# Performance work log

Measured on AMD Instinct MI355X. Metric: run time of the kernel, lower is better.

The kernel has to match this reference:

```python
import jax, jax.numpy as jnp
import numpy as np

N = 51200      # total nodes
E = 1638400    # total edges (avg degree 32)
G = 512        # graphs in batch
IN = 16        # input node features
H = 4          # heads
C = 32         # channels per head
HC = H * C     # 128, concat output width
SLOPE = 0.2    # LeakyReLU negative slope
BN_EPS = 1e-5


def _glorot(k, shape, fan):
    return jax.random.normal(k, shape, jnp.float32) / np.sqrt(fan).astype(np.float32)


def setup_inputs() -> dict:
    key = jax.random.key(0)
    ks = jax.random.split(key, 32)
    inp = {}
    inp['x'] = jax.random.normal(ks[0], (N, IN), jnp.float32)
    inp['edge_index'] = jax.random.randint(ks[1], (2, E), 0, N)
    inp['batch'] = jnp.sort(jax.random.randint(ks[2], (N,), 0, G))
    # GATv2 layer 1 (IN -> H*C)
    inp['l1_Wl'] = _glorot(ks[3], (IN, HC), IN)
    inp['l1_bl'] = jnp.zeros((HC,), jnp.float32)
    inp['l1_Wr'] = _glorot(ks[4], (IN, HC), IN)
    inp['l1_br'] = jnp.zeros((HC,), jnp.float32)
    inp['l1_att'] = _glorot(ks[5], (H, C), C)
    inp['l1_bias'] = jnp.zeros((HC,), jnp.float32)
    # GATv2 layer 2 (HC -> H*C)
    inp['l2_Wl'] = _glorot(ks[6], (HC, HC), HC)
    inp['l2_bl'] = jnp.zeros((HC,), jnp.float32)
    inp['l2_Wr'] = _glorot(ks[7], (HC, HC), HC)
    inp['l2_br'] = jnp.zeros((HC,), jnp.float32)
    inp['l2_att'] = _glorot(ks[8], (H, C), C)
    inp['l2_bias'] = jnp.zeros((HC,), jnp.float32)
    # MLP head (HC -> HC -> HC -> 2) with BatchNorm (eval mode, running stats 0/1)
    inp['fc1_W'] = _glorot(ks[9], (HC, HC), HC)
    inp['fc1_b'] = jnp.zeros((HC,), jnp.float32)
    inp['bn1_g'] = jnp.ones((HC,), jnp.float32)
    inp['bn1_b'] = jnp.zeros((HC,), jnp.float32)
    inp['fc2_W'] = _glorot(ks[10], (HC, HC), HC)
    inp['fc2_b'] = jnp.zeros((HC,), jnp.float32)
    inp['bn2_g'] = jnp.ones((HC,), jnp.float32)
    inp['bn2_b'] = jnp.zeros((HC,), jnp.float32)
    inp['fc3_W'] = _glorot(ks[11], (HC, 2), HC)
    inp['fc3_b'] = jnp.zeros((2,), jnp.float32)
    return inp


def gatv2_conv(x, src, dst, Wl, bl, Wr, br, att, bias):
    # PyG GATv2Conv (share_weights=False, concat=True), eval mode (no dropout).
    xl = (x @ Wl + bl).reshape(-1, H, C)  # source transform  [N,H,C]
    xr = (x @ Wr + br).reshape(-1, H, C)  # target transform  [N,H,C]
    e = jax.nn.leaky_relu(xl[src] + xr[dst], SLOPE)   # [E,H,C]
    score = jnp.einsum('ehc,hc->eh', e, att)          # [E,H]
    # segment softmax over edges sharing the same target node
    m = jax.ops.segment_max(score, dst, num_segments=N)
    ex = jnp.exp(score - m[dst])
    denom = jax.ops.segment_sum(ex, dst, num_segments=N)
    alpha = ex / (denom[dst] + 1e-16)                 # [E,H]
    out = jax.ops.segment_sum(xl[src] * alpha[:, :, None], dst, num_segments=N)
    return out.reshape(-1, HC) + bias


def reference(x, edge_index, batch,
              l1_Wl, l1_bl, l1_Wr, l1_br, l1_att, l1_bias,
              l2_Wl, l2_bl, l2_Wr, l2_br, l2_att, l2_bias,
              fc1_W, fc1_b, bn1_g, bn1_b,
              fc2_W, fc2_b, bn2_g, bn2_b,
              fc3_W, fc3_b):
    src, dst = edge_index[0], edge_index[1]
    h = jax.nn.relu(gatv2_conv(x, src, dst, l1_Wl, l1_bl, l1_Wr, l1_br, l1_att, l1_bias))
    h = jax.nn.relu(gatv2_conv(h, src, dst, l2_Wl, l2_bl, l2_Wr, l2_br, l2_att, l2_bias))
    # global mean pool over graphs
    s = jax.ops.segment_sum(h, batch, num_segments=G)
    cnt = jax.ops.segment_sum(jnp.ones((N,), h.dtype), batch, num_segments=G)
    g = s / jnp.maximum(cnt, 1.0)[:, None]            # [G,HC]
    # MLP head; BatchNorm1d in eval mode with running_mean=0, running_var=1
    def bn(z, gamma, beta):
        return z * (gamma / np.sqrt(1.0 + BN_EPS).astype(np.float32)) + beta
    g = jax.nn.relu(bn(g @ fc1_W + fc1_b, bn1_g, bn1_b))
    g = jax.nn.relu(bn(g @ fc2_W + fc2_b, bn2_g, bn2_b))
    return g @ fc3_W + fc3_b                          # [G,2]
```

## Files before the change

### kernel.cpp

```cpp
#include <hip/hip_runtime.h>
#include <math.h>

#define NN 51200
#define EE 1638400
#define GG 512
#define INF 16
#define HCC 128
#define NB 400
#define TILE 4096
#define NBLK (NN / 4)

typedef float vf2 __attribute__((ext_vector_type(2)));
typedef short v8s __attribute__((ext_vector_type(8)));
typedef float v4f __attribute__((ext_vector_type(4)));
#define FMA2 __builtin_elementwise_fma
#define MIN2 __builtin_elementwise_min
#define MAX2 __builtin_elementwise_max


__device__ __forceinline__ int wave_incl_scan(int v, int lane) {
#pragma unroll
    for (int d = 1; d < 64; d <<= 1) {
        int y = __shfl_up(v, d);
        if (lane >= d) v += y;
    }
    return v;
}

__device__ __forceinline__ unsigned short bf16_rtne(float f) {
    unsigned u = __builtin_bit_cast(unsigned, f);
    unsigned r = u + 0x7FFFu + ((u >> 16) & 1u);
    return (unsigned short)(r >> 16);
}

__global__ __launch_bounds__(256) void k_hist(const int* __restrict__ ei,
                                              int* __restrict__ bcnt) {
    __shared__ int h[NB];
    for (int i = threadIdx.x; i < NB; i += 256) h[i] = 0;
    __syncthreads();
    int e0 = blockIdx.x * TILE;
#pragma unroll
    for (int s = 0; s < 16; s++) {
        int d = ei[EE + e0 + s * 256 + threadIdx.x];
        atomicAdd(&h[d >> 7], 1);
    }
    __syncthreads();
    for (int i = threadIdx.x; i < NB; i += 256)
        if (h[i]) atomicAdd(&bcnt[i], h[i]);
}

__global__ __launch_bounds__(512) void k_scan2(const int* __restrict__ bcnt,
                                               int* __restrict__ bbase,
                                               int* __restrict__ gcur,
                                               int* __restrict__ rowptr) {
    __shared__ int sc[512];
    int t = threadIdx.x;
    int v = (t < NB) ? bcnt[t] : 0;
    sc[t] = v;
    __syncthreads();
    for (int off = 1; off < 512; off <<= 1) {
        int u = (t >= off) ? sc[t - off] : 0;
        __syncthreads();
        sc[t] += u;
        __syncthreads();
    }
    if (t < NB) { int ex = sc[t] - v; bbase[t] = ex; gcur[t] = ex; }
    if (t == 0) { bbase[NB] = EE; rowptr[NN] = EE; }
}

__global__ __launch_bounds__(512) void k_binlin1(const int* __restrict__ ei,
                                                 int* __restrict__ gcur,
                                                 unsigned* __restrict__ binned,
                                                 const float* __restrict__ x,
                                                 const float* __restrict__ Wl,
                                                 const float* __restrict__ bl,
                                                 const float* __restrict__ Wr,
                                                 const float* __restrict__ br,
                                                 float* __restrict__ xl,
                                                 float* __restrict__ xr,
                                                 const float* __restrict__ W2l,
                                                 const float* __restrict__ W2r,
                                                 unsigned short* __restrict__ Bhi,
                                                 unsigned short* __restrict__ Blo) {
    __shared__ int h[512];
    __shared__ int lexcl[NB], lcur[NB], baseg[NB];
    __shared__ unsigned stage[TILE];
    __shared__ int wsum[8];
    __shared__ float sx[4][INF];
    int t = threadIdx.x;
    if (blockIdx.x < NB) {
        int lane = t & 63, w = t >> 6;
        h[t] = 0;
        __syncthreads();
        int e0 = blockIdx.x * TILE;
        int sv[8], dv[8];
#pragma unroll
        for (int s = 0; s < 8; s++) {
            int e = e0 + s * 512 + t;
            sv[s] = ei[e];
            dv[s] = ei[EE + e];
            atomicAdd(&h[dv[s] >> 7], 1);
        }
        __syncthreads();
        int myh = h[t];
        int incl = wave_incl_scan(myh, lane);
        if (lane == 63) wsum[w] = incl;
        __syncthreads();
        int woff = 0;
        for (int i = 0; i < w; i++) woff += wsum[i];
        incl += woff;
        if (t < NB) {
            int ex = incl - myh;
            lexcl[t] = ex;
            lcur[t] = ex;
            baseg[t] = atomicAdd(&gcur[t], myh);
        }
        __syncthreads();
#pragma unroll
        for (int s = 0; s < 8; s++) {
            int b = dv[s] >> 7;
            int r = atomicAdd(&lcur[b], 1);
            stage[r] = (unsigned)sv[s] | ((unsigned)dv[s] << 16);
        }
        __syncthreads();
#pragma unroll
        for (int s = 0; s < 8; s++) {
            int idx = s * 512 + t;
            unsigned p = stage[idx];
            int b = (int)(p >> 23);
            binned[baseg[b] + idx - lexcl[b]] = p;
        }
    } else if (blockIdx.x < NB + NN / 4) {
        int bid = blockIdx.x - NB;
        int j = t & 127;
        int ty = t >> 7;
        int row = bid * 4 + ty;
        if (t < 64) {
            sx[t >> 4][t & 15] = x[(size_t)(bid * 4 + (t >> 4)) * INF + (t & 15)];
        }
        __syncthreads();
        float al = bl[j], ar = br[j];
#pragma unroll
        for (int k = 0; k < INF; k++) {
            float xv = sx[ty][k];
            al = fmaf(xv, Wl[k * HCC + j], al);
            ar = fmaf(xv, Wr[k * HCC + j], ar);
        }
        size_t s = ((size_t)(j >> 5) * NN + row) * 32 + (j & 31);
        xl[s] = al;
        xr[s] = ar;
    } else {
        int gt = (blockIdx.x - NB - NN / 4) * 512 + t;
        int ks = gt >> 10;
        int rem = gt & 1023;
        int nt = rem >> 6;
        int lane = rem & 63;
        int n = nt * 16 + (lane & 15);
        int kbase = ks * 32 + (lane >> 4) * 8;
        const float* src = (n < 128) ? (W2l + n) : (W2r + n - 128);
        unsigned short hi8[8], lo8[8];
#pragma unroll
        for (int j = 0; j < 8; j++) {
            float v = src[(size_t)(kbase + j) * HCC];
            unsigned short hb = bf16_rtne(v);
            float hf = __builtin_bit_cast(float, (unsigned)hb << 16);
            hi8[j] = hb;
            lo8[j] = bf16_rtne(v - hf);
        }
        size_t idx = (size_t)gt * 8;
#pragma unroll
        for (int j = 0; j < 8; j++) { Bhi[idx + j] = hi8[j]; Blo[idx + j] = lo8[j]; }
    }
}

__global__ __launch_bounds__(256) void k_csr(const unsigned* __restrict__ binned,
                                             const int* __restrict__ bbase,
                                             int* __restrict__ rowptr,
                                             int* __restrict__ col) {
    int b = blockIdx.x;
    int base = bbase[b];
    int cnt = bbase[b + 1] - base;
    __shared__ int nh[1024], ncur[1024];
    __shared__ int wsum[4];
    int t = threadIdx.x;
    int lane = t & 63, w = t >> 6;
#pragma unroll
    for (int i = 0; i < 4; i++) nh[t + 256 * i] = 0;
    __syncthreads();
    for (int e = t; e < cnt; e += 256) {
        unsigned p = binned[base + e];
        unsigned src = p & 0xFFFFu;
        int key = (int)(((p >> 16) & 127u) << 3) | (int)(src >> 13);
        atomicAdd(&nh[key], 1);
    }
    __syncthreads();
    int c0 = nh[4 * t + 0], c1 = nh[4 * t + 1], c2 = nh[4 * t + 2], c3 = nh[4 * t + 3];
    int tot = ((c0 + c1) + (c2 + c3));
    int incl = wave_incl_scan(tot, lane);
    if (lane == 63) wsum[w] = incl;
    __syncthreads();
    int woff = 0;
    for (int i = 0; i < w; i++) woff += wsum[i];
    int tex = incl + woff - tot;
    ncur[4 * t + 0] = base + tex;
    ncur[4 * t + 1] = base + tex + c0;
    ncur[4 * t + 2] = base + tex + c0 + c1;
    ncur[4 * t + 3] = base + tex + c0 + c1 + c2;
    if ((t & 1) == 0) rowptr[(b << 7) + (t >> 1)] = base + tex;
    __syncthreads();
    for (int e = t; e < cnt; e += 256) {
        unsigned p = binned[base + e];
        unsigned src = p & 0xFFFFu;
        int key = (int)(((p >> 16) & 127u) << 3) | (int)(src >> 13);
        int r = atomicAdd(&ncur[key], 1);
        col[r] = (int)src;
    }
}

__global__ __launch_bounds__(256) void k_lin2(const float* __restrict__ hin,
                                              const unsigned short* __restrict__ Bhi,
                                              const unsigned short* __restrict__ Blo,
                                              const float* __restrict__ bl,
                                              const float* __restrict__ br,
                                              float* __restrict__ outl,
                                              float* __restrict__ outr) {
    const int tid = threadIdx.x;
    const int wv = tid >> 6;
    const int lane = tid & 63;
    const int m = lane & 15;
    const int quad = lane >> 4;
    const int r0 = blockIdx.x * 64 + wv * 16;
    const float* arow = hin + (size_t)(r0 + m) * HCC + quad * 8;
    const v8s* bh = (const v8s*)Bhi;
    const v8s* bo = (const v8s*)Blo;

    v4f acc[16];
#pragma unroll
    for (int nt = 0; nt < 16; nt++) acc[nt] = (v4f){0.f, 0.f, 0.f, 0.f};

#pragma unroll
    for (int ks = 0; ks < 4; ks++) {
        const float4 av0 = *(const float4*)(arow + ks * 32);
        const float4 av1 = *(const float4*)(arow + ks * 32 + 4);
        const float af[8] = {av0.x, av0.y, av0.z, av0.w, av1.x, av1.y, av1.z, av1.w};
        v8s ahi, alo;
#pragma unroll
        for (int e = 0; e < 8; e++) {
            unsigned short hb = bf16_rtne(af[e]);
            float hf = __builtin_bit_cast(float, (unsigned)hb << 16);
            ahi[e] = (short)hb;
            alo[e] = (short)bf16_rtne(af[e] - hf);
        }
        const int base = ks * 16 * 64 + lane;
#pragma unroll
        for (int nt = 0; nt < 16; nt++) {
            v8s bhv = bh[base + nt * 64];
            v8s blv = bo[base + nt * 64];
            acc[nt] = __builtin_amdgcn_mfma_f32_16x16x32_bf16(ahi, bhv, acc[nt], 0, 0, 0);
            acc[nt] = __builtin_amdgcn_mfma_f32_16x16x32_bf16(ahi, blv, acc[nt], 0, 0, 0);
            acc[nt] = __builtin_amdgcn_mfma_f32_16x16x32_bf16(alo, bhv, acc[nt], 0, 0, 0);
        }
    }
#pragma unroll
    for (int nt = 0; nt < 16; nt++) {
        int n = nt * 16 + m;
        int c = n & 127;
        float bv = (n < 128) ? bl[c] : br[c];
        float* outp = ((n < 128) ? outl : outr) + (size_t)(c >> 5) * NN * 32 + (c & 31);
#pragma unroll
        for (int r = 0; r < 4; r++) {
            int row = r0 + quad * 4 + r;
            outp[(size_t)row * 32] = acc[nt][r] + bv;
        }
    }
}

__global__ __launch_bounds__(256) void k_attn(const int* __restrict__ rowptr,
                                              const int* __restrict__ col,
                                              const float* __restrict__ xl,
                                              const float* __restrict__ xr,
                                              const float* __restrict__ att,
                                              const float* __restrict__ bias,
                                              float* __restrict__ hout) {
    const int wave = threadIdx.x >> 6;
    const int lane = threadIdx.x & 63;
    const int sub = lane >> 3;
    const int hl = (lane >> 2) & 1;
    const int hq = lane & 3;
    const int pair = blockIdx.x / NBLK;
    const int n = (blockIdx.x - pair * NBLK) * 4 + wave;
    const int head = 2 * pair + hl;

    const float* xlh = xl + (size_t)head * NN * 32;
    const float* xrp = xr + ((size_t)head * NN + n) * 32 + hq * 8;
    const float4 xrv0 = *(const float4*)(xrp);
    const float4 xrv1 = *(const float4*)(xrp + 4);
    const float4 at0 = *(const float4*)(att + head * 32 + hq * 8);
    const float4 at1 = *(const float4*)(att + head * 32 + hq * 8 + 4);
    const vf2 xr01 = {xrv0.x, xrv0.y}, xr23 = {xrv0.z, xrv0.w};
    const vf2 xr45 = {xrv1.x, xrv1.y}, xr67 = {xrv1.z, xrv1.w};
    const vf2 at01 = {at0.x, at0.y}, at23 = {at0.z, at0.w};
    const vf2 at45 = {at1.x, at1.y}, at67 = {at1.z, at1.w};
    const vf2 Z2 = {0.f, 0.f}, C2 = {0.2f, 0.2f};
    const unsigned choff = (unsigned)hq * 32u;

    const int base = rowptr[n];
    const int deg = rowptr[n + 1] - base;

    float m = -INFINITY, l = 0.f;
    vf2 a01 = Z2, a23 = Z2, a45 = Z2, a67 = Z2;

    for (int i0 = 0; i0 < deg; i0 += 64) {
        int mye = 0;
        if (i0 + lane < deg) mye = col[base + i0 + lane];
        const int cnt = min(64, deg - i0);
        const int events = (cnt + 15) >> 4;
        for (int g = 0; g < events; ++g) {
            float4 v0[2], v1[2];
            float p[2];
#pragma unroll
            for (int k = 0; k < 2; ++k) {
                const int src = __shfl(mye, 16 * g + 8 * k + sub);
                const unsigned voff = ((unsigned)src << 7) + choff;
                v0[k] = *(const float4*)((const char*)xlh + voff);
                v1[k] = *(const float4*)((const char*)xlh + voff + 16);
            }
#pragma unroll
            for (int k = 0; k < 2; ++k) {
                const vf2 v01 = {v0[k].x, v0[k].y}, v23 = {v0[k].z, v0[k].w};
                const vf2 v45 = {v1[k].x, v1[k].y}, v67 = {v1[k].z, v1[k].w};
                vf2 e, kk, p2;
                e = v01 + xr01; kk = FMA2(C2, MIN2(e, Z2), MAX2(e, Z2)); p2 = kk * at01;
                e = v23 + xr23; kk = FMA2(C2, MIN2(e, Z2), MAX2(e, Z2)); p2 = FMA2(kk, at23, p2);
                e = v45 + xr45; kk = FMA2(C2, MIN2(e, Z2), MAX2(e, Z2)); p2 = FMA2(kk, at45, p2);
                e = v67 + xr67; kk = FMA2(C2, MIN2(e, Z2), MAX2(e, Z2)); p2 = FMA2(kk, at67, p2);
                float pp = p2.x + p2.y;
                pp += __shfl_xor(pp, 1);
                pp += __shfl_xor(pp, 2);
                if ((16 * g + 8 * k + sub) >= cnt) pp = -INFINITY;
                p[k] = pp;
            }
            float pm = fmaxf(p[0], p[1]);
            pm = fmaxf(pm, __shfl_xor(pm, 8));
            pm = fmaxf(pm, __shfl_xor(pm, 16));
            pm = fmaxf(pm, __shfl_xor(pm, 32));
            const float mn = fmaxf(m, pm);
            const float sc = __expf(m - mn);
            const float w0 = __expf(p[0] - mn);
            const float w1 = __expf(p[1] - mn);
            l = fmaf(l, sc, w0 + w1);
            const vf2 S = {sc, sc}, W0 = {w0, w0}, W1 = {w1, w1};
            const vf2 u01 = {v0[0].x, v0[0].y}, u23 = {v0[0].z, v0[0].w};
            const vf2 u45 = {v1[0].x, v1[0].y}, u67 = {v1[0].z, v1[0].w};
            const vf2 t01 = {v0[1].x, v0[1].y}, t23 = {v0[1].z, v0[1].w};
            const vf2 t45 = {v1[1].x, v1[1].y}, t67 = {v1[1].z, v1[1].w};
            a01 = FMA2(W1, t01, FMA2(W0, u01, a01 * S));
            a23 = FMA2(W1, t23, FMA2(W0, u23, a23 * S));
            a45 = FMA2(W1, t45, FMA2(W0, u45, a45 * S));
            a67 = FMA2(W1, t67, FMA2(W0, u67, a67 * S));
            m = mn;
        }
    }
    l += __shfl_xor(l, 8);
    l += __shfl_xor(l, 16);
    l += __shfl_xor(l, 32);
    float af[8] = {a01.x, a01.y, a23.x, a23.y, a45.x, a45.y, a67.x, a67.y};
#pragma unroll
    for (int i = 0; i < 8; i++) {
        af[i] += __shfl_xor(af[i], 8);
        af[i] += __shfl_xor(af[i], 16);
        af[i] += __shfl_xor(af[i], 32);
    }
    const float inv = 1.f / (l + 1e-16f);
    if (sub == 0) {
        const float4 b0 = *(const float4*)(bias + head * 32 + hq * 8);
        const float4 b1 = *(const float4*)(bias + head * 32 + hq * 8 + 4);
        float4 o0, o1;
        o0.x = fmaxf(fmaf(af[0], inv, b0.x), 0.f);
        o0.y = fmaxf(fmaf(af[1], inv, b0.y), 0.f);
        o0.z = fmaxf(fmaf(af[2], inv, b0.z), 0.f);
        o0.w = fmaxf(fmaf(af[3], inv, b0.w), 0.f);
        o1.x = fmaxf(fmaf(af[4], inv, b1.x), 0.f);
        o1.y = fmaxf(fmaf(af[5], inv, b1.y), 0.f);
        o1.z = fmaxf(fmaf(af[6], inv, b1.z), 0.f);
        o1.w = fmaxf(fmaf(af[7], inv, b1.w), 0.f);
        float* hp = hout + (size_t)n * HCC + head * 32 + hq * 8;
        *(float4*)(hp) = o0;
        *(float4*)(hp + 4) = o1;
    }
}

__global__ __launch_bounds__(128) void k_head(const float* __restrict__ h,
                                              const int* __restrict__ batch,
                                              const float* __restrict__ fc1W, const float* __restrict__ fc1b,
                                              const float* __restrict__ bn1g, const float* __restrict__ bn1b,
                                              const float* __restrict__ fc2W, const float* __restrict__ fc2b,
                                              const float* __restrict__ bn2g, const float* __restrict__ bn2b,
                                              const float* __restrict__ fc3W, const float* __restrict__ fc3b,
                                              float* __restrict__ out) {
    int g = blockIdx.x;
    int j = threadIdx.x;
    __shared__ float buf[HCC], buf2[HCC];
    int lo = 0, hi = NN;
    while (lo < hi) { int mid = (lo + hi) >> 1; if (batch[mid] < g) lo = mid + 1; else hi = mid; }
    int s = lo;
    lo = 0; hi = NN;
    while (lo < hi) { int mid = (lo + hi) >> 1; if (batch[mid] < g + 1) lo = mid + 1; else hi = mid; }
    int e = lo;
    float s0 = 0.f, s1 = 0.f, s2 = 0.f, s3 = 0.f;
    int n = s;
    for (; n + 3 < e; n += 4) {
        s0 += h[(size_t)n * HCC + j];
        s1 += h[(size_t)(n + 1) * HCC + j];
        s2 += h[(size_t)(n + 2) * HCC + j];
        s3 += h[(size_t)(n + 3) * HCC + j];
    }
    for (; n < e; n++) s0 += h[(size_t)n * HCC + j];
    float sum = (s0 + s1) + (s2 + s3);
    float cnt = (float)(e - s);
    buf[j] = sum / fmaxf(cnt, 1.0f);
    __syncthreads();
    const float SQ = 1.00000499998749994f;
    float a = fc1b[j];
    for (int k = 0; k < HCC; k++) a = fmaf(buf[k], fc1W[k * HCC + j], a);
    a = fmaf(a, bn1g[j] / SQ, bn1b[j]);
    a = fmaxf(a, 0.f);
    buf2[j] = a;
    __syncthreads();
    a = fc2b[j];
    for (int k = 0; k < HCC; k++) a = fmaf(buf2[k], fc2W[k * HCC + j], a);
    a = fmaf(a, bn2g[j] / SQ, bn2b[j]);
    a = fmaxf(a, 0.f);
    buf[j] = a;
    __syncthreads();
    if (j < 2) {
        float o = fc3b[j];
        for (int k = 0; k < HCC; k++) o = fmaf(buf[k], fc3W[k * 2 + j], o);
        out[g * 2 + j] = o;
    }
}

extern "C" void kernel_launch(void* const* d_in, const int* in_sizes, int n_in,
                              void* d_out, int out_size, void* d_ws, size_t ws_size,
                              hipStream_t stream) {
    const float* x      = (const float*)d_in[0];
    const int*   ei     = (const int*)d_in[1];
    const int*   batch  = (const int*)d_in[2];
    const float* l1_Wl  = (const float*)d_in[3];
    const float* l1_bl  = (const float*)d_in[4];
    const float* l1_Wr  = (const float*)d_in[5];
    const float* l1_br  = (const float*)d_in[6];
    const float* l1_att = (const float*)d_in[7];
    const float* l1_bias= (const float*)d_in[8];
    const float* l2_Wl  = (const float*)d_in[9];
    const float* l2_bl  = (const float*)d_in[10];
    const float* l2_Wr  = (const float*)d_in[11];
    const float* l2_br  = (const float*)d_in[12];
    const float* l2_att = (const float*)d_in[13];
    const float* l2_bias= (const float*)d_in[14];
    const float* fc1_W  = (const float*)d_in[15];
    const float* fc1_b  = (const float*)d_in[16];
    const float* bn1_g  = (const float*)d_in[17];
    const float* bn1_b  = (const float*)d_in[18];
    const float* fc2_W  = (const float*)d_in[19];
    const float* fc2_b  = (const float*)d_in[20];
    const float* bn2_g  = (const float*)d_in[21];
    const float* bn2_b  = (const float*)d_in[22];
    const float* fc3_W  = (const float*)d_in[23];
    const float* fc3_b  = (const float*)d_in[24];
    float* out = (float*)d_out;

    float* xl = (float*)d_ws;
    float* xr = xl + (size_t)NN * HCC;
    float* h  = xr + (size_t)NN * HCC;
    int* rowptr = (int*)(h + (size_t)NN * HCC);
    int* col    = rowptr + (NN + 1);
    int* bcnt   = col + EE;
    int* bbase  = bcnt + NB;
    int* gcur   = bbase + (NB + 1);
    uintptr_t bp = ((uintptr_t)(gcur + NB) + 15) & ~(uintptr_t)15;
    unsigned short* Bhi = (unsigned short*)bp;
    unsigned short* Blo = Bhi + 32768;
    unsigned* binned = (unsigned*)h;

    hipMemsetAsync(bcnt, 0, NB * sizeof(int), stream);
    k_hist<<<EE / TILE, 256, 0, stream>>>(ei, bcnt);
    k_scan2<<<1, 512, 0, stream>>>(bcnt, bbase, gcur, rowptr);
    k_binlin1<<<NB + NN / 4 + 8, 512, 0, stream>>>(ei, gcur, binned,
                                                   x, l1_Wl, l1_bl, l1_Wr, l1_br, xl, xr,
                                                   l2_Wl, l2_Wr, Bhi, Blo);
    k_csr<<<NB, 256, 0, stream>>>(binned, bbase, rowptr, col);

    k_attn<<<2 * NBLK, 256, 0, stream>>>(rowptr, col, xl, xr, l1_att, l1_bias, h);

    k_lin2<<<NN / 64, 256, 0, stream>>>(h, Bhi, Blo, l2_bl, l2_br, xl, xr);
    k_attn<<<2 * NBLK, 256, 0, stream>>>(rowptr, col, xl, xr, l2_att, l2_bias, h);

    k_head<<<GG, 128, 0, stream>>>(h, batch, fc1_W, fc1_b, bn1_g, bn1_b,
                                   fc2_W, fc2_b, bn2_g, bn2_b, fc3_W, fc3_b, out);
}
```

Before: 449.4 us.

## Halve CSR bucket width, cache binned edges in LDS, split head pooling

The edge-binning pipeline now uses 800 buckets of 64 destination nodes with 2048-edge tiles instead of 400 buckets of 128 nodes. This doubles the number of blocks in the binning and CSR-build kernels and shrinks their per-block work. The CSR kernel also stages up to 3072 binned edges in shared memory so its second pass skips a global re-read, falling back to global memory for overflow. The head kernel uses 256 threads so two halves split the mean-pool node loop, at the cost of idle threads in the MLP stages.

```diff
diff --git a/kernel.cpp b/kernel.cpp
--- a/kernel.cpp
+++ b/kernel.cpp
@@ -6,8 +6,9 @@
 #define GG 512
 #define INF 16
 #define HCC 128
-#define NB 400
-#define TILE 4096
+#define NB2 800
+#define TILE2 2048
+#define CSRCAP 3072
 #define NBLK (NN / 4)
 
 typedef float vf2 __attribute__((ext_vector_type(2)));
@@ -35,17 +36,17 @@
 
 __global__ __launch_bounds__(256) void k_hist(const int* __restrict__ ei,
                                               int* __restrict__ bcnt) {
-    __shared__ int h[NB];
-    for (int i = threadIdx.x; i < NB; i += 256) h[i] = 0;
-    __syncthreads();
-    int e0 = blockIdx.x * TILE;
-#pragma unroll
-    for (int s = 0; s < 16; s++) {
+    __shared__ int h[NB2];
+    for (int i = threadIdx.x; i < NB2; i += 256) h[i] = 0;
+    __syncthreads();
+    int e0 = blockIdx.x * TILE2;
+#pragma unroll
+    for (int s = 0; s < 8; s++) {
         int d = ei[EE + e0 + s * 256 + threadIdx.x];
-        atomicAdd(&h[d >> 7], 1);
-    }
-    __syncthreads();
-    for (int i = threadIdx.x; i < NB; i += 256)
+        atomicAdd(&h[d >> 6], 1);
+    }
+    __syncthreads();
+    for (int i = threadIdx.x; i < NB2; i += 256)
         if (h[i]) atomicAdd(&bcnt[i], h[i]);
 }
 
@@ -53,19 +54,23 @@
                                                int* __restrict__ bbase,
                                                int* __restrict__ gcur,
                                                int* __restrict__ rowptr) {
-    __shared__ int sc[512];
+    __shared__ int wsum[8];
     int t = threadIdx.x;
-    int v = (t < NB) ? bcnt[t] : 0;
-    sc[t] = v;
-    __syncthreads();
-    for (int off = 1; off < 512; off <<= 1) {
-        int u = (t >= off) ? sc[t - off] : 0;
-        __syncthreads();
-        sc[t] += u;
-        __syncthreads();
-    }
-    if (t < NB) { int ex = sc[t] - v; bbase[t] = ex; gcur[t] = ex; }
-    if (t == 0) { bbase[NB] = EE; rowptr[NN] = EE; }
+    int lane = t & 63, w = t >> 6;
+    int c0 = 0, c1 = 0;
+    if (t < NB2 / 2) { c0 = bcnt[2 * t]; c1 = bcnt[2 * t + 1]; }
+    int tot = c0 + c1;
+    int incl = wave_incl_scan(tot, lane);
+    if (lane == 63) wsum[w] = incl;
+    __syncthreads();
+    int woff = 0;
+    for (int i = 0; i < w; i++) woff += wsum[i];
+    int ex = incl + woff - tot;
+    if (t < NB2 / 2) {
+        bbase[2 * t] = ex;     gcur[2 * t] = ex;
+        bbase[2 * t + 1] = ex + c0; gcur[2 * t + 1] = ex + c0;
+    }
+    if (t == 0) { bbase[NB2] = EE; rowptr[NN] = EE; }
 }
 
 __global__ __launch_bounds__(512) void k_binlin1(const int* __restrict__ ei,
@@ -82,56 +87,58 @@
                                                  const float* __restrict__ W2r,
                                                  unsigned short* __restrict__ Bhi,
                                                  unsigned short* __restrict__ Blo) {
-    __shared__ int h[512];
-    __shared__ int lexcl[NB], lcur[NB], baseg[NB];
-    __shared__ unsigned stage[TILE];
+    __shared__ int lexcl[NB2], lcur[NB2], baseg[NB2];
+    __shared__ unsigned stage[TILE2];
     __shared__ int wsum[8];
     __shared__ float sx[4][INF];
     int t = threadIdx.x;
-    if (blockIdx.x < NB) {
+    if (blockIdx.x < NB2) {
         int lane = t & 63, w = t >> 6;
-        h[t] = 0;
-        __syncthreads();
-        int e0 = blockIdx.x * TILE;
-        int sv[8], dv[8];
-#pragma unroll
-        for (int s = 0; s < 8; s++) {
+        for (int i = t; i < NB2; i += 512) lcur[i] = 0;
+        __syncthreads();
+        int e0 = blockIdx.x * TILE2;
+        int sv[4], dv[4];
+#pragma unroll
+        for (int s = 0; s < 4; s++) {
             int e = e0 + s * 512 + t;
             sv[s] = ei[e];
             dv[s] = ei[EE + e];
-            atomicAdd(&h[dv[s] >> 7], 1);
-        }
-        __syncthreads();
-        int myh = h[t];
-        int incl = wave_incl_scan(myh, lane);
+            atomicAdd(&lcur[dv[s] >> 6], 1);
+        }
+        __syncthreads();
+        int c0 = 0, c1 = 0;
+        if (t < NB2 / 2) { c0 = lcur[2 * t]; c1 = lcur[2 * t + 1]; }
+        int tot = c0 + c1;
+        int incl = wave_incl_scan(tot, lane);
         if (lane == 63) wsum[w] = incl;
         __syncthreads();
         int woff = 0;
         for (int i = 0; i < w; i++) woff += wsum[i];
-        incl += woff;
-        if (t < NB) {
-            int ex = incl - myh;
-            lexcl[t] = ex;
-            lcur[t] = ex;
-            baseg[t] = atomicAdd(&gcur[t], myh);
-        }
-        __syncthreads();
-#pragma unroll
-        for (int s = 0; s < 8; s++) {
-            int b = dv[s] >> 7;
+        int ex = incl + woff - tot;
+        __syncthreads();
+        if (t < NB2 / 2) {
+            lexcl[2 * t] = ex;          lcur[2 * t] = ex;
+            lexcl[2 * t + 1] = ex + c0; lcur[2 * t + 1] = ex + c0;
+            baseg[2 * t] = atomicAdd(&gcur[2 * t], c0);
+            baseg[2 * t + 1] = atomicAdd(&gcur[2 * t + 1], c1);
+        }
+        __syncthreads();
+#pragma unroll
+        for (int s = 0; s < 4; s++) {
+            int b = dv[s] >> 6;
             int r = atomicAdd(&lcur[b], 1);
             stage[r] = (unsigned)sv[s] | ((unsigned)dv[s] << 16);
         }
         __syncthreads();
 #pragma unroll
-        for (int s = 0; s < 8; s++) {
+        for (int s = 0; s < 4; s++) {
             int idx = s * 512 + t;
             unsigned p = stage[idx];
-            int b = (int)(p >> 23);
+            int b = (int)(p >> 22);
             binned[baseg[b] + idx - lexcl[b]] = p;
         }
-    } else if (blockIdx.x < NB + NN / 4) {
-        int bid = blockIdx.x - NB;
+    } else if (blockIdx.x < NB2 + NN / 4) {
+        int bid = blockIdx.x - NB2;
         int j = t & 127;
         int ty = t >> 7;
         int row = bid * 4 + ty;
@@ -150,7 +157,7 @@
         xl[s] = al;
         xr[s] = ar;
     } else {
-        int gt = (blockIdx.x - NB - NN / 4) * 512 + t;
+        int gt = (blockIdx.x - NB2 - NN / 4) * 512 + t;
         int ks = gt >> 10;
         int rem = gt & 1023;
         int nt = rem >> 6;
@@ -180,38 +187,38 @@
     int b = blockIdx.x;
     int base = bbase[b];
     int cnt = bbase[b + 1] - base;
-    __shared__ int nh[1024], ncur[1024];
+    __shared__ int nh[512], ncur[512];
+    __shared__ unsigned sbin[CSRCAP];
     __shared__ int wsum[4];
     int t = threadIdx.x;
     int lane = t & 63, w = t >> 6;
-#pragma unroll
-    for (int i = 0; i < 4; i++) nh[t + 256 * i] = 0;
+    nh[t] = 0;
+    nh[t + 256] = 0;
     __syncthreads();
     for (int e = t; e < cnt; e += 256) {
         unsigned p = binned[base + e];
+        if (e < CSRCAP) sbin[e] = p;
         unsigned src = p & 0xFFFFu;
-        int key = (int)(((p >> 16) & 127u) << 3) | (int)(src >> 13);
+        int key = (int)(((p >> 16) & 63u) << 3) | (int)(src >> 13);
         atomicAdd(&nh[key], 1);
     }
     __syncthreads();
-    int c0 = nh[4 * t + 0], c1 = nh[4 * t + 1], c2 = nh[4 * t + 2], c3 = nh[4 * t + 3];
-    int tot = ((c0 + c1) + (c2 + c3));
+    int c0 = nh[2 * t], c1 = nh[2 * t + 1];
+    int tot = c0 + c1;
     int incl = wave_incl_scan(tot, lane);
     if (lane == 63) wsum[w] = incl;
     __syncthreads();
     int woff = 0;
     for (int i = 0; i < w; i++) woff += wsum[i];
     int tex = incl + woff - tot;
-    ncur[4 * t + 0] = base + tex;
-    ncur[4 * t + 1] = base + tex + c0;
-    ncur[4 * t + 2] = base + tex + c0 + c1;
-    ncur[4 * t + 3] = base + tex + c0 + c1 + c2;
-    if ((t & 1) == 0) rowptr[(b << 7) + (t >> 1)] = base + tex;
+    ncur[2 * t] = base + tex;
+    ncur[2 * t + 1] = base + tex + c0;
+    if ((t & 3) == 0) rowptr[(b << 6) + (t >> 2)] = base + tex;
     __syncthreads();
     for (int e = t; e < cnt; e += 256) {
-        unsigned p = binned[base + e];
+        unsigned p = (e < CSRCAP) ? sbin[e] : binned[base + e];
         unsigned src = p & 0xFFFFu;
-        int key = (int)(((p >> 16) & 127u) << 3) | (int)(src >> 13);
+        int key = (int)(((p >> 16) & 63u) << 3) | (int)(src >> 13);
         int r = atomicAdd(&ncur[key], 1);
         col[r] = (int)src;
     }
@@ -390,7 +397,7 @@
     }
 }
 
-__global__ __launch_bounds__(128) void k_head(const float* __restrict__ h,
+__global__ __launch_bounds__(256) void k_head(const float* __restrict__ h,
                                               const int* __restrict__ batch,
                                               const float* __restrict__ fc1W, const float* __restrict__ fc1b,
                                               const float* __restrict__ bn1g, const float* __restrict__ bn1b,
@@ -399,7 +406,10 @@
                                               const float* __restrict__ fc3W, const float* __restrict__ fc3b,
                                               float* __restrict__ out) {
     int g = blockIdx.x;
-    int j = threadIdx.x;
+    int t = threadIdx.x;
+    int j = t & 127;
+    int half = t >> 7;
+    __shared__ float part[256];
     __shared__ float buf[HCC], buf2[HCC];
     int lo = 0, hi = NN;
     while (lo < hi) { int mid = (lo + hi) >> 1; if (batch[mid] < g) lo = mid + 1; else hi = mid; }
@@ -408,35 +418,43 @@
     while (lo < hi) { int mid = (lo + hi) >> 1; if (batch[mid] < g + 1) lo = mid + 1; else hi = mid; }
     int e = lo;
     float s0 = 0.f, s1 = 0.f, s2 = 0.f, s3 = 0.f;
-    int n = s;
-    for (; n + 3 < e; n += 4) {
+    int n = s + half;
+    for (; n + 6 < e; n += 8) {
         s0 += h[(size_t)n * HCC + j];
-        s1 += h[(size_t)(n + 1) * HCC + j];
-        s2 += h[(size_t)(n + 2) * HCC + j];
-        s3 += h[(size_t)(n + 3) * HCC + j];
-    }
-    for (; n < e; n++) s0 += h[(size_t)n * HCC + j];
-    float sum = (s0 + s1) + (s2 + s3);
+        s1 += h[(size_t)(n + 2) * HCC + j];
+        s2 += h[(size_t)(n + 4) * HCC + j];
+        s3 += h[(size_t)(n + 6) * HCC + j];
+    }
+    for (; n < e; n += 2) s0 += h[(size_t)n * HCC + j];
+    part[t] = (s0 + s1) + (s2 + s3);
+    __syncthreads();
     float cnt = (float)(e - s);
-    buf[j] = sum / fmaxf(cnt, 1.0f);
+    if (t < 128) buf[j] = (part[j] + part[j + 128]) / fmaxf(cnt, 1.0f);
     __syncthreads();
     const float SQ = 1.00000499998749994f;
-    float a = fc1b[j];
-    for (int k = 0; k < HCC; k++) a = fmaf(buf[k], fc1W[k * HCC + j], a);
-    a = fmaf(a, bn1g[j] / SQ, bn1b[j]);
-    a = fmaxf(a, 0.f);
-    buf2[j] = a;
-    __syncthreads();
-    a = fc2b[j];
-    for (int k = 0; k < HCC; k++) a = fmaf(buf2[k], fc2W[k * HCC + j], a);
-    a = fmaf(a, bn2g[j] / SQ, bn2b[j]);
-    a = fmaxf(a, 0.f);
-    buf[j] = a;
-    __syncthreads();
-    if (j < 2) {
-        float o = fc3b[j];
-        for (int k = 0; k < HCC; k++) o = fmaf(buf[k], fc3W[k * 2 + j], o);
-        out[g * 2 + j] = o;
+    float a = 0.f;
+    if (t < 128) {
+        a = fc1b[j];
+        for (int k = 0; k < HCC; k++) a = fmaf(buf[k], fc1W[k * HCC + j], a);
+        a = fmaf(a, bn1g[j] / SQ, bn1b[j]);
+        a = fmaxf(a, 0.f);
+    }
+    __syncthreads();
+    if (t < 128) buf2[j] = a;
+    __syncthreads();
+    if (t < 128) {
+        a = fc2b[j];
+        for (int k = 0; k < HCC; k++) a = fmaf(buf2[k], fc2W[k * HCC + j], a);
+        a = fmaf(a, bn2g[j] / SQ, bn2b[j]);
+        a = fmaxf(a, 0.f);
+    }
+    __syncthreads();
+    if (t < 128) buf[j] = a;
+    __syncthreads();
+    if (t < 2) {
+        float o = fc3b[t];
+        for (int k = 0; k < HCC; k++) o = fmaf(buf[k], fc3W[k * 2 + t], o);
+        out[g * 2 + t] = o;
     }
 }
 
@@ -476,26 +494,26 @@
     int* rowptr = (int*)(h + (size_t)NN * HCC);
     int* col    = rowptr + (NN + 1);
     int* bcnt   = col + EE;
-    int* bbase  = bcnt + NB;
-    int* gcur   = bbase + (NB + 1);
-    uintptr_t bp = ((uintptr_t)(gcur + NB) + 15) & ~(uintptr_t)15;
+    int* bbase  = bcnt + NB2;
+    int* gcur   = bbase + (NB2 + 1);
+    uintptr_t bp = ((uintptr_t)(gcur + NB2) + 15) & ~(uintptr_t)15;
     unsigned short* Bhi = (unsigned short*)bp;
     unsigned short* Blo = Bhi + 32768;
     unsigned* binned = (unsigned*)h;
 
-    hipMemsetAsync(bcnt, 0, NB * sizeof(int), stream);
-    k_hist<<<EE / TILE, 256, 0, stream>>>(ei, bcnt);
+    hipMemsetAsync(bcnt, 0, NB2 * sizeof(int), stream);
+    k_hist<<<EE / TILE2, 256, 0, stream>>>(ei, bcnt);
     k_scan2<<<1, 512, 0, stream>>>(bcnt, bbase, gcur, rowptr);
-    k_binlin1<<<NB + NN / 4 + 8, 512, 0, stream>>>(ei, gcur, binned,
-                                                   x, l1_Wl, l1_bl, l1_Wr, l1_br, xl, xr,
-                                                   l2_Wl, l2_Wr, Bhi, Blo);
-    k_csr<<<NB, 256, 0, stream>>>(binned, bbase, rowptr, col);
+    k_binlin1<<<NB2 + NN / 4 + 8, 512, 0, stream>>>(ei, gcur, binned,
+                                                    x, l1_Wl, l1_bl, l1_Wr, l1_br, xl, xr,
+                                                    l2_Wl, l2_Wr, Bhi, Blo);
+    k_csr<<<NB2, 256, 0, stream>>>(binned, bbase, rowptr, col);
 
     k_attn<<<2 * NBLK, 256, 0, stream>>>(rowptr, col, xl, xr, l1_att, l1_bias, h);
 
     k_lin2<<<NN / 64, 256, 0, stream>>>(h, Bhi, Blo, l2_bl, l2_br, xl, xr);
     k_attn<<<2 * NBLK, 256, 0, stream>>>(rowptr, col, xl, xr, l2_att, l2_bias, h);
 
-    k_head<<<GG, 128, 0, stream>>>(h, batch, fc1_W, fc1_b, bn1_g, bn1_b,
+    k_head<<<GG, 256, 0, stream>>>(h, batch, fc1_W, fc1_b, bn1_g, bn1_b,
                                    fc2_W, fc2_b, bn2_g, bn2_b, fc3_W, fc3_b, out);
 }
```

After: 482.8 us. +7.4%, slower.
